# Kernel optimization log

Measured on AMD Instinct MI355X. Metric: run time of the kernel, lower is better.

Reference implementation:

```python
import jax, jax.numpy as jnp
import numpy as np

B, N, CIN, COUT = 32, 2048, 64, 128
BN_EPS = 1e-5
ADJ_EPS = 1e-6


def setup_inputs() -> dict:
    key = jax.random.key(0)
    k0, k1, k2 = jax.random.split(key, 3)
    x = jax.random.normal(k0, (B, N, CIN), dtype=jnp.float32)
    # adjacency: nonnegative weights, like an attention/affinity graph
    A = jax.random.uniform(k1, (B, N, N), dtype=jnp.float32)
    # 1x1 conv == pointwise linear over channels
    W = jax.random.normal(k2, (COUT, CIN), dtype=jnp.float32) * 0.05
    b = jnp.zeros((COUT,), dtype=jnp.float32)
    gamma = jnp.ones((COUT,), dtype=jnp.float32)
    beta = jnp.zeros((COUT,), dtype=jnp.float32)
    return {"x": x, "A": A, "W": W, "b": b, "gamma": gamma, "beta": beta}


def reference(x, A, W, b, gamma, beta):
    # Row-normalize each batch adjacency: A[i] / (A[i].sum(dim=1, keepdim=True) + eps)
    A_norm = A / (jnp.sum(A, axis=2, keepdims=True) + ADJ_EPS)  # [B,N,N]
    # Batched graph aggregation: xg[b,c,m] = sum_n x[b,n,c] * A_norm[b,n,m]
    xg = jnp.einsum('bnc,bnm->bcm', x, A_norm)  # [B,C,N]
    # 1x1 conv (pointwise channel mix)
    h = jnp.einsum('bcm,oc->bom', xg, W) + b[None, :, None]  # [B,COUT,N]
    # BatchNorm2d in training mode: batch stats over (B, spatial) per channel,
    # biased variance (as PyTorch uses for normalization)
    mean = jnp.mean(h, axis=(0, 2), keepdims=True)
    var = jnp.mean((h - mean) ** 2, axis=(0, 2), keepdims=True)
    hn = (h - mean) * jax.lax.rsqrt(var + BN_EPS)
    hn = hn * gamma[None, :, None] + beta[None, :, None]
    out = jax.nn.relu(hn)
    # permute(0,2,1,3).squeeze(-1) -> [B, N, COUT]
    return jnp.transpose(out, (0, 2, 1))
```

## Files before the change

### kernel.cpp

```cpp
#include <hip/hip_runtime.h>

#define NB   32
#define NN   2048
#define CINx 64
#define COUTx 128
#define ADJ_EPS 1e-6f
#define BN_EPS  1e-5f

#define XS_LEN  ((size_t)NB * NN * CINx)
#define BN1_OFF (XS_LEN)
#define BN2_OFF (XS_LEN + 128)
#define SC_OFF  (XS_LEN + 256)
#define SH_OFF  (XS_LEN + 384)

__global__ __launch_bounds__(256) void k1_rowsum(const float* __restrict__ A,
                                                 const float* __restrict__ x,
                                                 float* __restrict__ xs) {
    int row  = blockIdx.x * 4 + (threadIdx.x >> 6);
    int lane = threadIdx.x & 63;
    const float4* a4 = reinterpret_cast<const float4*>(A + (size_t)row * NN);
    float s = 0.f;
#pragma unroll
    for (int i = 0; i < 8; ++i) {
        float4 v = a4[i * 64 + lane];
        s += (v.x + v.y) + (v.z + v.w);
    }
#pragma unroll
    for (int off = 32; off > 0; off >>= 1) s += __shfl_down(s, off);
    float inv = 1.f / (__shfl(s, 0) + ADJ_EPS);
    xs[(size_t)row * CINx + lane] = x[(size_t)row * CINx + lane] * inv;
}

#define FMA4(d, s, v)                    \
    d.x = fmaf(s, v.x, d.x);             \
    d.y = fmaf(s, v.y, d.y);             \
    d.z = fmaf(s, v.z, d.z);             \
    d.w = fmaf(s, v.w, d.w)

__global__ __launch_bounds__(256, 2) void k2_gemm(const float* __restrict__ A,
                                                  const float* __restrict__ xs,
                                                  const float* __restrict__ W,
                                                  const float* __restrict__ bias,
                                                  float* __restrict__ hout,
                                                  float* __restrict__ bnsum,
                                                  float* __restrict__ bnsumsq) {
    __shared__ float Atile[64 * 128];
    __shared__ float XSt[64 * 64];
    __shared__ float bn1[256], bn2[256];

    int b  = blockIdx.x & 31;
    int m0 = (blockIdx.x >> 5) * 128;
    int t  = threadIdx.x;

    float4 acc[8];
#pragma unroll
    for (int i = 0; i < 8; ++i) acc[i] = make_float4(0.f, 0.f, 0.f, 0.f);

    const int ml = (t & 31) * 4;
    const int c0 = (t >> 5) * 8;

    for (int n0 = 0; n0 < NN; n0 += 64) {
        __syncthreads();
#pragma unroll
        for (int i = 0; i < 8; ++i) {
            int idx = t + i * 256;
            int r = idx >> 5, c4 = (idx & 31) * 4;
            *reinterpret_cast<float4*>(&Atile[r * 128 + c4]) =
                *reinterpret_cast<const float4*>(
                    &A[((size_t)b * NN + n0 + r) * NN + m0 + c4]);
        }
#pragma unroll
        for (int i = 0; i < 4; ++i) {
            int idx = t + i * 256;
            int r = idx >> 4, c4 = (idx & 15) * 4;
            *reinterpret_cast<float4*>(&XSt[r * 64 + c4]) =
                *reinterpret_cast<const float4*>(
                    &xs[((size_t)b * NN + n0 + r) * CINx + c4]);
        }
        __syncthreads();
#pragma unroll 8
        for (int kk = 0; kk < 64; ++kk) {
            float4 am = *reinterpret_cast<const float4*>(&Atile[kk * 128 + ml]);
            float4 xa = *reinterpret_cast<const float4*>(&XSt[kk * 64 + c0]);
            float4 xb = *reinterpret_cast<const float4*>(&XSt[kk * 64 + c0 + 4]);
            FMA4(acc[0], xa.x, am);
            FMA4(acc[1], xa.y, am);
            FMA4(acc[2], xa.z, am);
            FMA4(acc[3], xa.w, am);
            FMA4(acc[4], xb.x, am);
            FMA4(acc[5], xb.y, am);
            FMA4(acc[6], xb.z, am);
            FMA4(acc[7], xb.w, am);
        }
    }
    __syncthreads();
#pragma unroll
    for (int cc = 0; cc < 8; ++cc)
        *reinterpret_cast<float4*>(&Atile[(c0 + cc) * 128 + ml]) = acc[cc];
    __syncthreads();

    int o  = t & 127;
    int mq = t >> 7;
    const float* Wrow = W + o * 64;
    float bo = bias[o];
    float s1 = 0.f, s2 = 0.f;
    for (int mc = 0; mc < 4; ++mc) {
        float h[16];
#pragma unroll
        for (int i = 0; i < 16; ++i) h[i] = bo;
        for (int c = 0; c < 64; ++c) {
            float w = Wrow[c];
            const float* xgp = &Atile[c * 128 + mq * 64 + mc * 16];
            float4 g0 = *reinterpret_cast<const float4*>(&xgp[0]);
            float4 g1 = *reinterpret_cast<const float4*>(&xgp[4]);
            float4 g2 = *reinterpret_cast<const float4*>(&xgp[8]);
            float4 g3 = *reinterpret_cast<const float4*>(&xgp[12]);
            h[0]  = fmaf(w, g0.x, h[0]);  h[1]  = fmaf(w, g0.y, h[1]);
            h[2]  = fmaf(w, g0.z, h[2]);  h[3]  = fmaf(w, g0.w, h[3]);
            h[4]  = fmaf(w, g1.x, h[4]);  h[5]  = fmaf(w, g1.y, h[5]);
            h[6]  = fmaf(w, g1.z, h[6]);  h[7]  = fmaf(w, g1.w, h[7]);
            h[8]  = fmaf(w, g2.x, h[8]);  h[9]  = fmaf(w, g2.y, h[9]);
            h[10] = fmaf(w, g2.z, h[10]); h[11] = fmaf(w, g2.w, h[11]);
            h[12] = fmaf(w, g3.x, h[12]); h[13] = fmaf(w, g3.y, h[13]);
            h[14] = fmaf(w, g3.z, h[14]); h[15] = fmaf(w, g3.w, h[15]);
        }
        size_t base = ((size_t)b * NN + m0 + mq * 64 + mc * 16) * COUTx + o;
#pragma unroll
        for (int i = 0; i < 16; ++i) {
            float v = h[i];
            s1 += v;
            s2 = fmaf(v, v, s2);
            hout[base + (size_t)i * COUTx] = v;
        }
    }
    bn1[t] = s1;
    bn2[t] = s2;
    __syncthreads();
    if (t < 128) {
        atomicAdd(&bnsum[o],   bn1[t] + bn1[t + 128]);
        atomicAdd(&bnsumsq[o], bn2[t] + bn2[t + 128]);
    }
}

__global__ void k3_bnstats(const float* __restrict__ bnsum,
                           const float* __restrict__ bnsumsq,
                           const float* __restrict__ gamma,
                           const float* __restrict__ beta,
                           float* __restrict__ scale,
                           float* __restrict__ shift) {
    int o = threadIdx.x;
    if (o < COUTx) {
        const float invn = 1.f / ((float)NB * (float)NN);
        float mean = bnsum[o] * invn;
        float var  = bnsumsq[o] * invn - mean * mean;
        float sc   = gamma[o] * rsqrtf(var + BN_EPS);
        scale[o] = sc;
        shift[o] = beta[o] - mean * sc;
    }
}

__global__ __launch_bounds__(256) void k4_bnapply(float* __restrict__ hout,
                                                  const float* __restrict__ scale,
                                                  const float* __restrict__ shift) {
    const float4* sc4 = reinterpret_cast<const float4*>(scale);
    const float4* sh4 = reinterpret_cast<const float4*>(shift);
    float4* h4 = reinterpret_cast<float4*>(hout);
    const size_t n4 = (size_t)NB * NN * COUTx / 4;
    for (size_t idx = (size_t)blockIdx.x * blockDim.x + threadIdx.x; idx < n4;
         idx += (size_t)gridDim.x * blockDim.x) {
        int o4 = (int)(idx & 31);
        float4 h = h4[idx];
        float4 s = sc4[o4];
        float4 f = sh4[o4];
        h.x = fmaxf(fmaf(h.x, s.x, f.x), 0.f);
        h.y = fmaxf(fmaf(h.y, s.y, f.y), 0.f);
        h.z = fmaxf(fmaf(h.z, s.z, f.z), 0.f);
        h.w = fmaxf(fmaf(h.w, s.w, f.w), 0.f);
        h4[idx] = h;
    }
}

extern "C" void kernel_launch(void* const* d_in, const int* in_sizes, int n_in,
                              void* d_out, int out_size, void* d_ws, size_t ws_size,
                              hipStream_t stream) {
    const float* x     = (const float*)d_in[0];
    const float* A     = (const float*)d_in[1];
    const float* W     = (const float*)d_in[2];
    const float* bvec  = (const float*)d_in[3];
    const float* gamma = (const float*)d_in[4];
    const float* beta  = (const float*)d_in[5];
    float* out = (float*)d_out;
    float* ws  = (float*)d_ws;

    float* xs      = ws;
    float* bnsum   = ws + BN1_OFF;
    float* bnsumsq = ws + BN2_OFF;
    float* scale   = ws + SC_OFF;
    float* shift   = ws + SH_OFF;

    hipMemsetAsync(bnsum, 0, 256 * sizeof(float), stream);

    k1_rowsum<<<NB * NN / 4, 256, 0, stream>>>(A, x, xs);
    k2_gemm<<<NB * (NN / 128), 256, 0, stream>>>(A, xs, W, bvec, out, bnsum, bnsumsq);
    k3_bnstats<<<1, 128, 0, stream>>>(bnsum, bnsumsq, gamma, beta, scale, shift);
    k4_bnapply<<<2048, 256, 0, stream>>>(out, scale, shift);
}
```

Baseline: 981.1 us.

## Use bf16 MFMA for graph aggregation with transposed bf16 normalized features

Replaces the FP32 FMA main GEMM with bf16 MFMA 16x16x32 instructions. A is converted to bf16 into a transposed LDS tile, and k1 now writes the normalized x as a channel-major bf16 array. The pointwise conv weights are also stored as bf16 in shared memory. This targets the compute-bound FP32 inner loop, at the cost of bf16 precision on A, x and W, and of scalar strided A loads for the transpose.

Measured after the change: 833.5 us. -15.1%, faster.

```diff
diff --git a/kernel.cpp b/kernel.cpp
--- a/kernel.cpp
+++ b/kernel.cpp
@@ -2,135 +2,205 @@
 
 #define NB   32
 #define NN   2048
-#define CINx 64
-#define COUTx 128
+#define CIN  64
+#define COUT 128
 #define ADJ_EPS 1e-6f
 #define BN_EPS  1e-5f
 
-#define XS_LEN  ((size_t)NB * NN * CINx)
-#define BN1_OFF (XS_LEN)
-#define BN2_OFF (XS_LEN + 128)
-#define SC_OFF  (XS_LEN + 256)
-#define SH_OFF  (XS_LEN + 384)
-
-__global__ __launch_bounds__(256) void k1_rowsum(const float* __restrict__ A,
-                                                 const float* __restrict__ x,
-                                                 float* __restrict__ xs) {
-    int row  = blockIdx.x * 4 + (threadIdx.x >> 6);
-    int lane = threadIdx.x & 63;
-    const float4* a4 = reinterpret_cast<const float4*>(A + (size_t)row * NN);
-    float s = 0.f;
-#pragma unroll
-    for (int i = 0; i < 8; ++i) {
-        float4 v = a4[i * 64 + lane];
-        s += (v.x + v.y) + (v.z + v.w);
-    }
-#pragma unroll
-    for (int off = 32; off > 0; off >>= 1) s += __shfl_down(s, off);
-    float inv = 1.f / (__shfl(s, 0) + ADJ_EPS);
-    xs[(size_t)row * CINx + lane] = x[(size_t)row * CINx + lane] * inv;
-}
-
-#define FMA4(d, s, v)                    \
-    d.x = fmaf(s, v.x, d.x);             \
-    d.y = fmaf(s, v.y, d.y);             \
-    d.z = fmaf(s, v.z, d.z);             \
-    d.w = fmaf(s, v.w, d.w)
+typedef __attribute__((ext_vector_type(8))) short short8;
+typedef __attribute__((ext_vector_type(4))) float floatx4;
+
+#define BN1_OFF 0
+#define BN2_OFF 128
+#define SC_OFF  256
+#define SH_OFF  384
+#define XST_OFF 512
+
+static __device__ __forceinline__ ushort f2bf(float f) {
+    union { float f; unsigned u; } v; v.f = f;
+    unsigned r = v.u + 0x7FFFu + ((v.u >> 16) & 1u);
+    return (ushort)(r >> 16);
+}
+static __device__ __forceinline__ float bf2f(ushort u) {
+    return __uint_as_float(((unsigned)u) << 16);
+}
+
+__global__ __launch_bounds__(256) void k1_norm(const float* __restrict__ A,
+                                               const float* __restrict__ x,
+                                               ushort* __restrict__ xsT) {
+    __shared__ float invr[128];
+    __shared__ __align__(16) ushort xsb[64 * 136];
+    int b  = blockIdx.x & 31;
+    int n0 = (blockIdx.x >> 5) * 128;
+    int t  = threadIdx.x;
+    int w  = t >> 6, lane = t & 63;
+
+    for (int i = 0; i < 32; i += 2) {
+        int r0 = w * 32 + i;
+        const float4* a0 = (const float4*)(A + ((size_t)b * NN + n0 + r0) * NN);
+        const float4* a1 = (const float4*)(A + ((size_t)b * NN + n0 + r0 + 1) * NN);
+        float s0 = 0.f, s1 = 0.f;
+#pragma unroll
+        for (int j = 0; j < 8; ++j) {
+            float4 v0 = a0[j * 64 + lane];
+            float4 v1 = a1[j * 64 + lane];
+            s0 += (v0.x + v0.y) + (v0.z + v0.w);
+            s1 += (v1.x + v1.y) + (v1.z + v1.w);
+        }
+#pragma unroll
+        for (int off = 32; off; off >>= 1) {
+            s0 += __shfl_down(s0, off);
+            s1 += __shfl_down(s1, off);
+        }
+        if (lane == 0) {
+            invr[r0]     = 1.f / (s0 + ADJ_EPS);
+            invr[r0 + 1] = 1.f / (s1 + ADJ_EPS);
+        }
+    }
+    __syncthreads();
+    {
+        int c = t & 63, nh = t >> 6;
+#pragma unroll
+        for (int i = 0; i < 16; ++i) {
+            int dn = nh * 32 + i * 2;
+            float x0 = x[((size_t)b * NN + n0 + dn) * CIN + c] * invr[dn];
+            float x1 = x[((size_t)b * NN + n0 + dn + 1) * CIN + c] * invr[dn + 1];
+            ushort2 p; p.x = f2bf(x0); p.y = f2bf(x1);
+            *(ushort2*)&xsb[c * 136 + dn] = p;
+        }
+    }
+    __syncthreads();
+    {
+        int c = t >> 2, s = t & 3;
+#pragma unroll
+        for (int i = 0; i < 4; ++i) {
+            short8 v = *(const short8*)&xsb[c * 136 + (s * 4 + i) * 8];
+            *(short8*)&xsT[((size_t)b * CIN + c) * NN + n0 + (s * 4 + i) * 8] = v;
+        }
+    }
+}
 
 __global__ __launch_bounds__(256, 2) void k2_gemm(const float* __restrict__ A,
-                                                  const float* __restrict__ xs,
+                                                  const ushort* __restrict__ xsT,
                                                   const float* __restrict__ W,
                                                   const float* __restrict__ bias,
                                                   float* __restrict__ hout,
                                                   float* __restrict__ bnsum,
                                                   float* __restrict__ bnsumsq) {
-    __shared__ float Atile[64 * 128];
-    __shared__ float XSt[64 * 64];
+    __shared__ __align__(16) ushort Att[128 * 72];
+    __shared__ __align__(16) ushort Xst[64 * 72];
+    __shared__ __align__(16) float  xg[64 * 128];
+    __shared__ __align__(16) ushort2 Wb[32 * 128];
     __shared__ float bn1[256], bn2[256];
 
     int b  = blockIdx.x & 31;
     int m0 = (blockIdx.x >> 5) * 128;
     int t  = threadIdx.x;
-
-    float4 acc[8];
-#pragma unroll
-    for (int i = 0; i < 8; ++i) acc[i] = make_float4(0.f, 0.f, 0.f, 0.f);
-
-    const int ml = (t & 31) * 4;
-    const int c0 = (t >> 5) * 8;
+    int w  = t >> 6, lane = t & 63;
+    int l15 = lane & 15, q = lane >> 4;
+
+    {
+        ushort* wbu = (ushort*)Wb;
+        int c = t & 63, o0 = (t >> 6) * 32;
+#pragma unroll
+        for (int p = 0; p < 32; ++p) {
+            int o = o0 + p;
+            wbu[(c >> 1) * 256 + o * 2 + (c & 1)] = f2bf(W[o * CIN + c]);
+        }
+    }
+
+    floatx4 acc[4][2];
+#pragma unroll
+    for (int ct = 0; ct < 4; ++ct)
+#pragma unroll
+        for (int j = 0; j < 2; ++j) {
+            floatx4 z = {0.f, 0.f, 0.f, 0.f};
+            acc[ct][j] = z;
+        }
 
     for (int n0 = 0; n0 < NN; n0 += 64) {
         __syncthreads();
-#pragma unroll
-        for (int i = 0; i < 8; ++i) {
-            int idx = t + i * 256;
-            int r = idx >> 5, c4 = (idx & 31) * 4;
-            *reinterpret_cast<float4*>(&Atile[r * 128 + c4]) =
-                *reinterpret_cast<const float4*>(
-                    &A[((size_t)b * NN + n0 + r) * NN + m0 + c4]);
-        }
-#pragma unroll
-        for (int i = 0; i < 4; ++i) {
-            int idx = t + i * 256;
-            int r = idx >> 4, c4 = (idx & 15) * 4;
-            *reinterpret_cast<float4*>(&XSt[r * 64 + c4]) =
-                *reinterpret_cast<const float4*>(
-                    &xs[((size_t)b * NN + n0 + r) * CINx + c4]);
+        {
+            int mm = t & 127, nh = t >> 7;
+            const float* Ab = A + ((size_t)b * NN + n0) * NN + m0 + mm;
+#pragma unroll
+            for (int i = 0; i < 16; ++i) {
+                int dn = nh * 32 + i * 2;
+                float a0 = Ab[(size_t)dn * NN];
+                float a1 = Ab[(size_t)(dn + 1) * NN];
+                ushort2 p; p.x = f2bf(a0); p.y = f2bf(a1);
+                *(ushort2*)&Att[mm * 72 + dn] = p;
+            }
+        }
+        {
+            int c = t >> 2, s = t & 3;
+#pragma unroll
+            for (int i = 0; i < 2; ++i) {
+                short8 v = *(const short8*)&xsT[((size_t)b * CIN + c) * NN + n0 + (s * 2 + i) * 8];
+                *(short8*)&Xst[c * 72 + (s * 2 + i) * 8] = v;
+            }
         }
         __syncthreads();
-#pragma unroll 8
-        for (int kk = 0; kk < 64; ++kk) {
-            float4 am = *reinterpret_cast<const float4*>(&Atile[kk * 128 + ml]);
-            float4 xa = *reinterpret_cast<const float4*>(&XSt[kk * 64 + c0]);
-            float4 xb = *reinterpret_cast<const float4*>(&XSt[kk * 64 + c0 + 4]);
-            FMA4(acc[0], xa.x, am);
-            FMA4(acc[1], xa.y, am);
-            FMA4(acc[2], xa.z, am);
-            FMA4(acc[3], xa.w, am);
-            FMA4(acc[4], xb.x, am);
-            FMA4(acc[5], xb.y, am);
-            FMA4(acc[6], xb.z, am);
-            FMA4(acc[7], xb.w, am);
-        }
-    }
-    __syncthreads();
-#pragma unroll
-    for (int cc = 0; cc < 8; ++cc)
-        *reinterpret_cast<float4*>(&Atile[(c0 + cc) * 128 + ml]) = acc[cc];
+#pragma unroll
+        for (int kk = 0; kk < 64; kk += 32) {
+            short8 af[4], bfr[2];
+#pragma unroll
+            for (int ct = 0; ct < 4; ++ct)
+                af[ct] = *(const short8*)&Xst[(ct * 16 + l15) * 72 + kk + q * 8];
+#pragma unroll
+            for (int j = 0; j < 2; ++j)
+                bfr[j] = *(const short8*)&Att[((w * 2 + j) * 16 + l15) * 72 + kk + q * 8];
+#pragma unroll
+            for (int ct = 0; ct < 4; ++ct)
+#pragma unroll
+                for (int j = 0; j < 2; ++j)
+                    acc[ct][j] = __builtin_amdgcn_mfma_f32_16x16x32_bf16(
+                        af[ct], bfr[j], acc[ct][j], 0, 0, 0);
+        }
+    }
+    __syncthreads();
+#pragma unroll
+    for (int ct = 0; ct < 4; ++ct)
+#pragma unroll
+        for (int j = 0; j < 2; ++j) {
+            int col = (w * 2 + j) * 16 + l15;
+#pragma unroll
+            for (int r = 0; r < 4; ++r)
+                xg[(ct * 16 + q * 4 + r) * 128 + col] = acc[ct][j][r];
+        }
     __syncthreads();
 
     int o  = t & 127;
     int mq = t >> 7;
-    const float* Wrow = W + o * 64;
     float bo = bias[o];
     float s1 = 0.f, s2 = 0.f;
     for (int mc = 0; mc < 4; ++mc) {
         float h[16];
 #pragma unroll
         for (int i = 0; i < 16; ++i) h[i] = bo;
-        for (int c = 0; c < 64; ++c) {
-            float w = Wrow[c];
-            const float* xgp = &Atile[c * 128 + mq * 64 + mc * 16];
-            float4 g0 = *reinterpret_cast<const float4*>(&xgp[0]);
-            float4 g1 = *reinterpret_cast<const float4*>(&xgp[4]);
-            float4 g2 = *reinterpret_cast<const float4*>(&xgp[8]);
-            float4 g3 = *reinterpret_cast<const float4*>(&xgp[12]);
-            h[0]  = fmaf(w, g0.x, h[0]);  h[1]  = fmaf(w, g0.y, h[1]);
-            h[2]  = fmaf(w, g0.z, h[2]);  h[3]  = fmaf(w, g0.w, h[3]);
-            h[4]  = fmaf(w, g1.x, h[4]);  h[5]  = fmaf(w, g1.y, h[5]);
-            h[6]  = fmaf(w, g1.z, h[6]);  h[7]  = fmaf(w, g1.w, h[7]);
-            h[8]  = fmaf(w, g2.x, h[8]);  h[9]  = fmaf(w, g2.y, h[9]);
-            h[10] = fmaf(w, g2.z, h[10]); h[11] = fmaf(w, g2.w, h[11]);
-            h[12] = fmaf(w, g3.x, h[12]); h[13] = fmaf(w, g3.y, h[13]);
-            h[14] = fmaf(w, g3.z, h[14]); h[15] = fmaf(w, g3.w, h[15]);
-        }
-        size_t base = ((size_t)b * NN + m0 + mq * 64 + mc * 16) * COUTx + o;
+#pragma unroll
+        for (int c2 = 0; c2 < 32; ++c2) {
+            ushort2 wp = Wb[c2 * 128 + o];
+            float w0 = bf2f(wp.x), w1 = bf2f(wp.y);
+            const float* x0p = &xg[(2 * c2) * 128 + mq * 64 + mc * 16];
+            const float* x1p = &xg[(2 * c2 + 1) * 128 + mq * 64 + mc * 16];
+#pragma unroll
+            for (int v = 0; v < 4; ++v) {
+                float4 g0 = *(const float4*)&x0p[v * 4];
+                float4 g1 = *(const float4*)&x1p[v * 4];
+                h[v * 4 + 0] = fmaf(w0, g0.x, fmaf(w1, g1.x, h[v * 4 + 0]));
+                h[v * 4 + 1] = fmaf(w0, g0.y, fmaf(w1, g1.y, h[v * 4 + 1]));
+                h[v * 4 + 2] = fmaf(w0, g0.z, fmaf(w1, g1.z, h[v * 4 + 2]));
+                h[v * 4 + 3] = fmaf(w0, g0.w, fmaf(w1, g1.w, h[v * 4 + 3]));
+            }
+        }
+        size_t base = ((size_t)b * NN + m0 + mq * 64 + mc * 16) * COUT + o;
 #pragma unroll
         for (int i = 0; i < 16; ++i) {
             float v = h[i];
             s1 += v;
             s2 = fmaf(v, v, s2);
-            hout[base + (size_t)i * COUTx] = v;
+            hout[base + (size_t)i * COUT] = v;
         }
     }
     bn1[t] = s1;
@@ -149,7 +219,7 @@
                            float* __restrict__ scale,
                            float* __restrict__ shift) {
     int o = threadIdx.x;
-    if (o < COUTx) {
+    if (o < COUT) {
         const float invn = 1.f / ((float)NB * (float)NN);
         float mean = bnsum[o] * invn;
         float var  = bnsumsq[o] * invn - mean * mean;
@@ -162,10 +232,10 @@
 __global__ __launch_bounds__(256) void k4_bnapply(float* __restrict__ hout,
                                                   const float* __restrict__ scale,
                                                   const float* __restrict__ shift) {
-    const float4* sc4 = reinterpret_cast<const float4*>(scale);
-    const float4* sh4 = reinterpret_cast<const float4*>(shift);
-    float4* h4 = reinterpret_cast<float4*>(hout);
-    const size_t n4 = (size_t)NB * NN * COUTx / 4;
+    const float4* sc4 = (const float4*)scale;
+    const float4* sh4 = (const float4*)shift;
+    float4* h4 = (float4*)hout;
+    const size_t n4 = (size_t)NB * NN * COUT / 4;
     for (size_t idx = (size_t)blockIdx.x * blockDim.x + threadIdx.x; idx < n4;
          idx += (size_t)gridDim.x * blockDim.x) {
         int o4 = (int)(idx & 31);
@@ -192,16 +262,16 @@
     float* out = (float*)d_out;
     float* ws  = (float*)d_ws;
 
-    float* xs      = ws;
-    float* bnsum   = ws + BN1_OFF;
-    float* bnsumsq = ws + BN2_OFF;
-    float* scale   = ws + SC_OFF;
-    float* shift   = ws + SH_OFF;
+    float*  bnsum   = ws + BN1_OFF;
+    float*  bnsumsq = ws + BN2_OFF;
+    float*  scale   = ws + SC_OFF;
+    float*  shift   = ws + SH_OFF;
+    ushort* xsT     = (ushort*)(ws + XST_OFF);
 
     hipMemsetAsync(bnsum, 0, 256 * sizeof(float), stream);
 
-    k1_rowsum<<<NB * NN / 4, 256, 0, stream>>>(A, x, xs);
-    k2_gemm<<<NB * (NN / 128), 256, 0, stream>>>(A, xs, W, bvec, out, bnsum, bnsumsq);
+    k1_norm<<<NB * (NN / 128), 256, 0, stream>>>(A, x, xsT);
+    k2_gemm<<<NB * (NN / 128), 256, 0, stream>>>(A, xsT, W, bvec, out, bnsum, bnsumsq);
     k3_bnstats<<<1, 128, 0, stream>>>(bnsum, bnsumsq, gamma, beta, scale, shift);
     k4_bnapply<<<2048, 256, 0, stream>>>(out, scale, shift);
 }
```
